# Kernel tuning notes

Hardware: AMD Instinct MI355X
Metric: run time of the kernel (lower is better)

## Reference

```python
import jax, jax.numpy as jnp
import numpy as np

MAX_SEQ = 512
HIDDEN = 1024
E = 2 * HIDDEN  # expansion
S = 128         # head dim s
EPS = 1e-5


def setup_inputs() -> dict:
    key = jax.random.key(0)
    ks = jax.random.split(key, 10)
    B, N = 32, 512
    x = jax.random.normal(ks[0], (B, N, HIDDEN), dtype=jnp.float32)
    attention_mask = jnp.ones((B, N), dtype=jnp.float32)
    gamma = jax.random.uniform(ks[1], (2, S), dtype=jnp.float32)
    beta = jax.random.uniform(ks[2], (2, S), dtype=jnp.float32)
    w = jax.random.uniform(ks[3], (2 * MAX_SEQ - 1,), dtype=jnp.float32)
    a_p = jax.random.uniform(ks[4], (1, S), dtype=jnp.float32)
    b_p = jax.random.uniform(ks[5], (1, S), dtype=jnp.float32)
    # uv: Linear(hidden -> 2e+s), stored input-major for x @ uv_w
    uv_w = jax.random.normal(ks[6], (HIDDEN, 2 * E + S), dtype=jnp.float32) * 0.02
    uv_b = jnp.zeros((2 * E + S,), dtype=jnp.float32)
    o_w = jax.random.normal(ks[7], (E, HIDDEN), dtype=jnp.float32) * 0.02
    o_b = jnp.zeros((HIDDEN,), dtype=jnp.float32)
    ln_g = jnp.ones((HIDDEN,), dtype=jnp.float32)
    ln_b = jnp.zeros((HIDDEN,), dtype=jnp.float32)
    return {"x": x, "attention_mask": attention_mask, "gamma": gamma, "beta": beta,
            "w": w, "a_p": a_p, "b_p": b_p, "uv_w": uv_w, "uv_b": uv_b,
            "o_w": o_w, "o_b": o_b, "ln_g": ln_g, "ln_b": ln_b}


def _rope_seq(x):
    # x: [b, n, 2, s]; rotary positions along axis 1 (matches module's rope(x, dim=1))
    n, d = x.shape[1], x.shape[-1]
    half = d // 2
    pos = jnp.arange(n, dtype=jnp.float32)
    # inv_freq = 10000 ** (arange(half)/half)  (freq_seq = -arange/half, inv = 10000**-freq_seq)
    inv_freq = jnp.power(10000.0, jnp.arange(half, dtype=jnp.float32) / half)
    sinusoid = pos[:, None] * inv_freq  # [n, half]
    sin = jnp.sin(sinusoid)[None, :, None, :]
    cos = jnp.cos(sinusoid)[None, :, None, :]
    x1, x2 = jnp.split(x, 2, axis=-1)
    return jnp.concatenate([x1 * cos - x2 * sin, x2 * cos + x1 * sin], axis=-1)


def _rel_pos_bias(w, seq_len):
    # Toeplitz trick (max_seq_length <= 512 path)
    t = jnp.pad(w[: 2 * MAX_SEQ - 1], (0, MAX_SEQ))          # [3S-1]
    t = jnp.tile(t, MAX_SEQ)[: -MAX_SEQ].reshape(-1, MAX_SEQ, 3 * MAX_SEQ - 2)
    r = (2 * MAX_SEQ - 1) // 2
    t = t[..., r:-r]                                          # [1, S, S]
    return t[:, :seq_len, :seq_len]


def reference(x, attention_mask, gamma, beta, w, a_p, b_p, uv_w, uv_b, o_w, o_b, ln_g, ln_b):
    n = x.shape[1]
    shortcut = x
    mu = jnp.mean(x, axis=-1, keepdims=True)
    var = jnp.mean(jnp.square(x - mu), axis=-1, keepdims=True)
    xn = (x - mu) * jax.lax.rsqrt(var + EPS) * ln_g + ln_b
    uv = jax.nn.silu(xn @ uv_w + uv_b)                        # [b, n, 2e+s]
    u, v, base = jnp.split(uv, [E, 2 * E], axis=-1)
    base = base[..., None, :] * gamma + beta                  # [b, n, 2, s]
    base = _rope_seq(base)
    q, k = base[:, :, 0], base[:, :, 1]                       # [b, n, s]
    qk = jnp.einsum('bnd,bmd->bnm', q, k)
    qk = qk + ((1.0 - attention_mask) * -1e12)[:, None, :]
    bias = _rel_pos_bias(w, n)                                # [1, n, n]
    kernel = jnp.square(jax.nn.relu(qk / MAX_SEQ + bias))
    out = u * jnp.einsum('bnm,bme->bne', kernel, v)           # [b, n, e]
    return out @ o_w + o_b + shortcut
```

## Files before the change

kernel.cpp:

```cpp
#include <hip/hip_runtime.h>
#include <math.h>

#define HIDDEN 1024
#define NSEQ   512
#define BATCH  32
#define EDIM   2048
#define SDIM   128
#define UVN    (2 * EDIM + SDIM)

using short8  = __attribute__((ext_vector_type(8))) short;
using float4x = __attribute__((ext_vector_type(4))) float;

__device__ __forceinline__ ushort f2bf(float f) {
    unsigned u = __float_as_uint(f);
    u += 0x7FFFu + ((u >> 16) & 1u);
    return (ushort)(u >> 16);
}
__device__ __forceinline__ float bf2f(ushort h) {
    return __uint_as_float(((unsigned)h) << 16);
}

#define ASYNC16(gp, lp) __builtin_amdgcn_global_load_lds( \
    (const __attribute__((address_space(1))) unsigned int*)(unsigned long long)(const void*)(gp), \
    (__attribute__((address_space(3))) unsigned int*)(unsigned int)(unsigned long long)(const void*)(lp), \
    16, 0, 0)

__global__ __launch_bounds__(64) void tab_kernel(float* __restrict__ sin_t,
                                                 float* __restrict__ cos_t) {
    int i = blockIdx.x;
    int j = threadIdx.x;
    double inv = pow(10000.0, (double)j / 64.0);
    double ang = (double)i * inv;
    sin_t[i * 64 + j] = (float)sin(ang);
    cos_t[i * 64 + j] = (float)cos(ang);
}

__global__ __launch_bounds__(256) void transpose_f32_bf16(const float* __restrict__ src,
                                                          ushort* __restrict__ dst,
                                                          int R, int Cc) {
    __shared__ float tile[32][33];
    const int bx = blockIdx.x;
    const int by = blockIdx.y;
    const int lx = threadIdx.x & 31;
    const int gy = threadIdx.x >> 5;
#pragma unroll
    for (int i = 0; i < 4; ++i) {
        int r = by * 32 + gy + i * 8;
        tile[gy + i * 8][lx] = src[(size_t)r * Cc + bx * 32 + lx];
    }
    __syncthreads();
#pragma unroll
    for (int i = 0; i < 4; ++i) {
        int c = bx * 32 + gy + i * 8;
        dst[(size_t)c * R + by * 32 + lx] = f2bf(tile[lx][gy + i * 8]);
    }
}

__global__ __launch_bounds__(256) void ln_kernel(const float* __restrict__ x,
                                                 const float* __restrict__ g,
                                                 const float* __restrict__ b,
                                                 ushort* __restrict__ xn) {
    const size_t t = blockIdx.x;
    const int tid = threadIdx.x;
    const float4 v = ((const float4*)(x + t * HIDDEN))[tid];
    float s = v.x + v.y + v.z + v.w;
#pragma unroll
    for (int off = 32; off > 0; off >>= 1) s += __shfl_down(s, off);
    __shared__ float red[4];
    const int wid = tid >> 6, lane = tid & 63;
    if (lane == 0) red[wid] = s;
    __syncthreads();
    const float mean = (red[0] + red[1] + red[2] + red[3]) * (1.0f / HIDDEN);
    __syncthreads();
    const float dx = v.x - mean, dy = v.y - mean, dz = v.z - mean, dw = v.w - mean;
    float s2 = dx * dx + dy * dy + dz * dz + dw * dw;
#pragma unroll
    for (int off = 32; off > 0; off >>= 1) s2 += __shfl_down(s2, off);
    if (lane == 0) red[wid] = s2;
    __syncthreads();
    const float var = (red[0] + red[1] + red[2] + red[3]) * (1.0f / HIDDEN);
    const float rs = rsqrtf(var + 1e-5f);
    const float4 gv = ((const float4*)g)[tid];
    const float4 bv = ((const float4*)b)[tid];
    ushort4 o;
    o.x = f2bf(dx * rs * gv.x + bv.x);
    o.y = f2bf(dy * rs * gv.y + bv.y);
    o.z = f2bf(dz * rs * gv.z + bv.z);
    o.w = f2bf(dw * rs * gv.w + bv.w);
    ((ushort4*)(xn + t * HIDDEN))[tid] = o;
}

__device__ __forceinline__ void mfma_core_128(const ushort* __restrict__ A,
                                              const ushort* __restrict__ Bt,
                                              const int lda, const int ldb, const int K,
                                              const int m0, const int n0,
                                              ushort* As, ushort* Bs,
                                              float4x (&acc)[4][4]) {
    const int tid = threadIdx.x;
    const int l = tid & 63, w = tid >> 6;
    const int wm = (w & 1) << 6, wn = (w >> 1) << 6;

    const int c0 = w * 128 + l;
    const int r0 = c0 >> 2, kc0 = (c0 & 3) * 8;
    const int c1 = c0 + 64;
    const int r1 = c1 >> 2, kc1 = (c1 & 3) * 8;
    char* ldsA0 = (char*)As + (size_t)(w * 128) * 16;
    char* ldsA1 = ldsA0 + 1024;
    char* ldsB0 = (char*)Bs + (size_t)(w * 128) * 16;
    char* ldsB1 = ldsB0 + 1024;
    const ushort* gA0 = A + (size_t)(m0 + r0) * lda + kc0;
    const ushort* gA1 = A + (size_t)(m0 + r1) * lda + kc1;
    const ushort* gB0 = Bt + (size_t)(n0 + r0) * ldb + kc0;
    const ushort* gB1 = Bt + (size_t)(n0 + r1) * ldb + kc1;

    const int lr = l & 15, lk = (l >> 4) * 8;
    int aoff[4], boff[4];
#pragma unroll
    for (int i = 0; i < 4; ++i) {
        aoff[i] = (wm + i * 16 + lr) * 32 + lk;
        boff[i] = (wn + i * 16 + lr) * 32 + lk;
    }

    for (int k0 = 0; k0 < K; k0 += 32) {
        __syncthreads();
        ASYNC16(gA0 + k0, ldsA0);
        ASYNC16(gA1 + k0, ldsA1);
        ASYNC16(gB0 + k0, ldsB0);
        ASYNC16(gB1 + k0, ldsB1);
        __syncthreads();
        short8 af[4], bfr[4];
#pragma unroll
        for (int i = 0; i < 4; ++i) af[i] = *(const short8*)(As + aoff[i]);
#pragma unroll
        for (int i = 0; i < 4; ++i) bfr[i] = *(const short8*)(Bs + boff[i]);
#pragma unroll
        for (int mi = 0; mi < 4; ++mi)
#pragma unroll
            for (int ni = 0; ni < 4; ++ni)
                acc[mi][ni] = __builtin_amdgcn_mfma_f32_16x16x32_bf16(
                    af[mi], bfr[ni], acc[mi][ni], 0, 0, 0);
    }
}

template <typename F>
__device__ __forceinline__ void epilogue_loop(const float4x (&acc)[4][4],
                                              int m0, int n0, F body) {
    const int l = threadIdx.x & 63, w = threadIdx.x >> 6;
    const int wm = (w & 1) << 6, wn = (w >> 1) << 6;
    const int lrow = (l >> 4) << 2, lcol = l & 15;
#pragma unroll
    for (int mi = 0; mi < 4; ++mi)
#pragma unroll
        for (int ni = 0; ni < 4; ++ni)
#pragma unroll
            for (int r = 0; r < 4; ++r) {
                const int m = m0 + wm + mi * 16 + lrow + r;
                const int n = n0 + wn + ni * 16 + lcol;
                body(m, n, acc[mi][ni][r]);
            }
}

__global__ __launch_bounds__(256) void gemm_uv_mfma(const ushort* __restrict__ A,
                                                    const ushort* __restrict__ Bt,
                                                    const float* __restrict__ bias,
                                                    ushort* __restrict__ U,
                                                    ushort* __restrict__ VT,
                                                    float* __restrict__ BASE) {
    __shared__ ushort As[128 * 32], Bs[128 * 32];
    float4x acc[4][4] = {};
    const int n0 = blockIdx.x * 128, m0 = blockIdx.y * 128;
    mfma_core_128(A, Bt, HIDDEN, HIDDEN, HIDDEN, m0, n0, As, Bs, acc);
    const int bx = blockIdx.x;
    if (bx < 16) {
        epilogue_loop(acc, m0, n0, [&](int m, int n, float aval) {
            float val = aval + bias[n];
            val = val / (1.0f + expf(-val));
            U[(size_t)m * EDIM + n] = f2bf(val);
        });
    } else if (bx < 32) {
        epilogue_loop(acc, m0, n0, [&](int m, int n, float aval) {
            float val = aval + bias[n];
            val = val / (1.0f + expf(-val));
            const int e = n - EDIM;
            const int b = m >> 9;
            const int s = m & (NSEQ - 1);
            VT[((size_t)b * EDIM + e) * NSEQ + s] = f2bf(val);
        });
    } else {
        epilogue_loop(acc, m0, n0, [&](int m, int n, float aval) {
            float val = aval + bias[n];
            val = val / (1.0f + expf(-val));
            BASE[(size_t)m * SDIM + (n - 2 * EDIM)] = val;
        });
    }
}

__global__ __launch_bounds__(128) void rope_kernel(const float* __restrict__ base,
                                                   const float* __restrict__ gamma,
                                                   const float* __restrict__ beta,
                                                   const float* __restrict__ sin_t,
                                                   const float* __restrict__ cos_t,
                                                   float* __restrict__ q,
                                                   float* __restrict__ k) {
    const size_t t = blockIdx.x;
    const int d = threadIdx.x;
    const int pos = (int)(t & (NSEQ - 1));
    __shared__ float vq[128], vk[128];
    const float bval = base[t * SDIM + d];
    vq[d] = bval * gamma[d] + beta[d];
    vk[d] = bval * gamma[SDIM + d] + beta[SDIM + d];
    __syncthreads();
    const int h = d & 63;
    const float sn = sin_t[pos * 64 + h];
    const float cs = cos_t[pos * 64 + h];
    float oq, ok;
    if (d < 64) {
        oq = vq[d] * cs - vq[d + 64] * sn;
        ok = vk[d] * cs - vk[d + 64] * sn;
    } else {
        oq = vq[d] * cs + vq[d - 64] * sn;
        ok = vk[d] * cs + vk[d - 64] * sn;
    }
    q[t * SDIM + d] = oq;
    k[t * SDIM + d] = ok;
}

__global__ __launch_bounds__(256) void gemm_qk(const float* __restrict__ q,
                                               const float* __restrict__ k,
                                               const float* __restrict__ mask,
                                               const float* __restrict__ w,
                                               ushort* __restrict__ km) {
    __shared__ float As[16][68];
    __shared__ float Bs[16][68];
    const int b = blockIdx.z;
    const float* A = q + (size_t)b * NSEQ * SDIM;
    const float* B = k + (size_t)b * NSEQ * SDIM;
    const int tid = threadIdx.x;
    const int tx = tid & 15, ty = tid >> 4;
    const int arow = tid >> 2, acol = (tid & 3) << 2;
    const int n0 = blockIdx.x * 64, m0 = blockIdx.y * 64;
    float acc[4][4] = {};
    for (int k0 = 0; k0 < SDIM; k0 += 16) {
        float4 av = *(const float4*)(A + (size_t)(m0 + arow) * SDIM + (k0 + acol));
        float4 bv = *(const float4*)(B + (size_t)(n0 + arow) * SDIM + (k0 + acol));
        As[acol + 0][arow] = av.x; As[acol + 1][arow] = av.y;
        As[acol + 2][arow] = av.z; As[acol + 3][arow] = av.w;
        Bs[acol + 0][arow] = bv.x; Bs[acol + 1][arow] = bv.y;
        Bs[acol + 2][arow] = bv.z; Bs[acol + 3][arow] = bv.w;
        __syncthreads();
#pragma unroll
        for (int kk = 0; kk < 16; ++kk) {
            const float4 a4 = *(const float4*)&As[kk][ty << 2];
            const float4 b4 = *(const float4*)&Bs[kk][tx << 2];
            const float a[4] = {a4.x, a4.y, a4.z, a4.w};
            const float bb[4] = {b4.x, b4.y, b4.z, b4.w};
#pragma unroll
            for (int i = 0; i < 4; ++i)
#pragma unroll
                for (int j = 0; j < 4; ++j)
                    acc[i][j] = fmaf(a[i], bb[j], acc[i][j]);
        }
        __syncthreads();
    }
    const float inv512 = 1.0f / 512.0f;
#pragma unroll
    for (int i = 0; i < 4; ++i) {
        const int ii = m0 + (ty << 2) + i;
#pragma unroll
        for (int j = 0; j < 4; ++j) {
            const int jj = n0 + (tx << 2) + j;
            const float mterm = (1.0f - mask[b * NSEQ + jj]) * -1e12f;
            float val = (acc[i][j] + mterm) * inv512 + w[511 + jj - ii];
            val = fmaxf(val, 0.0f);
            km[(size_t)b * NSEQ * NSEQ + (size_t)ii * NSEQ + jj] = f2bf(val * val);
        }
    }
}

__global__ __launch_bounds__(256) void gemm_pv_mfma(const ushort* __restrict__ km,
                                                    const ushort* __restrict__ vT,
                                                    ushort* __restrict__ ug) {
    __shared__ ushort As[128 * 32], Bs[128 * 32];
    float4x acc[4][4] = {};
    const int b = blockIdx.z;
    const int n0 = blockIdx.x * 128, m0 = blockIdx.y * 128;
    mfma_core_128(km + (size_t)b * NSEQ * NSEQ, vT + (size_t)b * EDIM * NSEQ,
                  NSEQ, NSEQ, NSEQ, m0, n0, As, Bs, acc);
    const size_t tokbase = (size_t)b * NSEQ;
    epilogue_loop(acc, m0, n0, [&](int m, int n, float aval) {
        const size_t idx = (tokbase + m) * EDIM + n;
        ug[idx] = f2bf(bf2f(ug[idx]) * aval);
    });
}

__global__ __launch_bounds__(256) void gemm_out_mfma(const ushort* __restrict__ A,
                                                     const ushort* __restrict__ Bt,
                                                     const float* __restrict__ ob,
                                                     const float* __restrict__ x,
                                                     float* __restrict__ out) {
    __shared__ ushort As[128 * 32], Bs[128 * 32];
    float4x acc[4][4] = {};
    const int n0 = blockIdx.x * 128, m0 = blockIdx.y * 128;
    mfma_core_128(A, Bt, EDIM, EDIM, EDIM, m0, n0, As, Bs, acc);
    epilogue_loop(acc, m0, n0, [&](int m, int n, float aval) {
        out[(size_t)m * HIDDEN + n] = aval + ob[n] + x[(size_t)m * HIDDEN + n];
    });
}

extern "C" void kernel_launch(void* const* d_in, const int* in_sizes, int n_in,
                              void* d_out, int out_size, void* d_ws, size_t ws_size,
                              hipStream_t stream) {
    const float* x     = (const float*)d_in[0];
    const float* mask  = (const float*)d_in[1];
    const float* gamma = (const float*)d_in[2];
    const float* beta  = (const float*)d_in[3];
    const float* w     = (const float*)d_in[4];
    const float* uv_w  = (const float*)d_in[7];
    const float* uv_b  = (const float*)d_in[8];
    const float* o_w   = (const float*)d_in[9];
    const float* o_b   = (const float*)d_in[10];
    const float* ln_g  = (const float*)d_in[11];
    const float* ln_b  = (const float*)d_in[12];
    float* out = (float*)d_out;

    int C = 32;
    while (C > 1) {
        unsigned long long need = (unsigned long long)C * 5505024ull + 13107200ull;
        if (need <= (unsigned long long)ws_size) break;
        C >>= 1;
    }
    const int R = C * NSEQ;

    char* p = (char*)d_ws;
    ushort* xn  = (ushort*)p;  p += (size_t)C * 1048576;
    ushort* u   = (ushort*)p;  p += (size_t)C * 2097152;
    ushort* vT  = (ushort*)p;  p += (size_t)C * 2097152;
    float* base = (float*)p;   p += (size_t)C * 262144;
    float* sint = (float*)p;   p += 131072;
    float* cost = (float*)p;   p += 131072;
    ushort* uv_wt = (ushort*)p; p += 8650752;
    ushort* o_wt  = (ushort*)p; p += 4194304;
    float* q  = (float*)xn;
    float* k  = (float*)((char*)xn + (size_t)C * 262144);
    ushort* km = (ushort*)((char*)xn + (size_t)C * 524288);

    hipLaunchKernelGGL(tab_kernel, dim3(512), dim3(64), 0, stream, sint, cost);
    hipLaunchKernelGGL(transpose_f32_bf16, dim3(132, 32), dim3(256), 0, stream,
                       uv_w, uv_wt, HIDDEN, UVN);
    hipLaunchKernelGGL(transpose_f32_bf16, dim3(32, 64), dim3(256), 0, stream,
                       o_w, o_wt, EDIM, HIDDEN);

    for (int b0 = 0; b0 < BATCH; b0 += C) {
        const float* xc = x + (size_t)b0 * NSEQ * HIDDEN;
        float*       oc = out + (size_t)b0 * NSEQ * HIDDEN;
        const float* mc = mask + (size_t)b0 * NSEQ;
        hipLaunchKernelGGL(ln_kernel, dim3(R), dim3(256), 0, stream, xc, ln_g, ln_b, xn);
        hipLaunchKernelGGL(gemm_uv_mfma, dim3(33, R / 128), dim3(256), 0, stream,
                           xn, uv_wt, uv_b, u, vT, base);
        hipLaunchKernelGGL(rope_kernel, dim3(R), dim3(128), 0, stream,
                           base, gamma, beta, sint, cost, q, k);
        hipLaunchKernelGGL(gemm_qk, dim3(8, 8, C), dim3(256), 0, stream, q, k, mc, w, km);
        hipLaunchKernelGGL(gemm_pv_mfma, dim3(16, 4, C), dim3(256), 0, stream, km, vT, u);
        hipLaunchKernelGGL(gemm_out_mfma, dim3(8, R / 128), dim3(256), 0, stream,
                           u, o_wt, o_b, xc, oc);
    }
}
```

Before: 607.9 us.

## Use 256x256 MFMA tiles with double-buffered async LDS pipeline for big GEMMs

Adds a 512-thread 256x256-tile bf16 MFMA core with K-step 64, double-buffered 128KB LDS, swizzled async global-to-LDS loads interleaved with four MFMA phases, and setprio hints. The UV, PV and output GEMMs switch to this core, and the small 128-column base projection is split into its own 128-tile kernel. The aim is more data reuse per LDS load and load latency hidden behind MFMA work. In exchange, the grids are much smaller (fewer blocks per launch) and register and LDS pressure rise.

```diff
diff --git a/kernel.cpp b/kernel.cpp
--- a/kernel.cpp
+++ b/kernel.cpp
@@ -160,25 +160,176 @@
             }
 }
 
-__global__ __launch_bounds__(256) void gemm_uv_mfma(const ushort* __restrict__ A,
-                                                    const ushort* __restrict__ Bt,
-                                                    const float* __restrict__ bias,
-                                                    ushort* __restrict__ U,
-                                                    ushort* __restrict__ VT,
-                                                    float* __restrict__ BASE) {
-    __shared__ ushort As[128 * 32], Bs[128 * 32];
-    float4x acc[4][4] = {};
-    const int n0 = blockIdx.x * 128, m0 = blockIdx.y * 128;
-    mfma_core_128(A, Bt, HIDDEN, HIDDEN, HIDDEN, m0, n0, As, Bs, acc);
-    const int bx = blockIdx.x;
-    if (bx < 16) {
-        epilogue_loop(acc, m0, n0, [&](int m, int n, float aval) {
+__device__ __forceinline__ void mfma_core_256(const ushort* __restrict__ A,
+                                              const ushort* __restrict__ Bt,
+                                              const int lda, const int ldb, const int K,
+                                              const int m0, const int n0,
+                                              char* smem,
+                                              float4x (&acc)[8][4]) {
+    const int tid = threadIdx.x;
+    const int l = tid & 63, w = tid >> 6;
+    const int wm = w >> 2, wn = w & 3;
+
+    const int srow = l >> 2;
+    const int kcol = (w & 1) * 32 + (((tid & 3) ^ ((l >> 3) & 3)) << 3);
+    const int rb0  = w >> 1;
+    const ushort* gA[4];
+    const ushort* gB[4];
+#pragma unroll
+    for (int j = 0; j < 4; ++j) {
+        const int row = (j * 4 + rb0) * 16 + srow;
+        gA[j] = A  + (size_t)(m0 + row) * lda + kcol;
+        gB[j] = Bt + (size_t)(n0 + row) * ldb + kcol;
+    }
+    char* const ldsA = smem;
+    char* const ldsB = smem + 65536;
+    const int wdst = w * 1024;
+
+#define STG_A(buf, j, t)  ASYNC16(gA[j] + (size_t)(t) * 64, ldsA + (buf) * 32768 + (j) * 8192 + wdst)
+#define STG_B(buf, j, t)  ASYNC16(gB[j] + (size_t)(t) * 64, ldsB + (buf) * 32768 + (j) * 8192 + wdst)
+#define RAWBAR() do { __builtin_amdgcn_sched_barrier(0); __builtin_amdgcn_s_barrier(); \
+                      __builtin_amdgcn_sched_barrier(0); } while (0)
+
+    const int LB = (l & 15) * 64 + (((l >> 4) ^ ((l >> 1) & 3)) << 4);
+    const int rbbA0 = wm * 4;
+    const int rbbA1 = 8 + wm * 4;
+    const int cbbB0 = wn * 2;
+    const int cbbB1 = 8 + wn * 2;
+
+    const int KT = K >> 6;
+
+    STG_A(0, 0, 0); STG_A(0, 1, 0); STG_A(0, 2, 0); STG_A(0, 3, 0);
+    STG_B(0, 0, 0); STG_B(0, 1, 0); STG_B(0, 2, 0); STG_B(0, 3, 0);
+    STG_A(1, 0, 1); STG_A(1, 1, 1); STG_B(1, 2, 1); STG_B(1, 3, 1);
+    asm volatile("s_waitcnt vmcnt(4)" ::: "memory");
+    RAWBAR();
+
+    for (int t = 0; t < KT; ++t) {
+        const int buf = t & 1, nbuf = buf ^ 1;
+        const char* Ab = ldsA + buf * 32768;
+        const char* Bb = ldsB + buf * 32768;
+        short8 a[4][2], bb[2][2];
+
+#pragma unroll
+        for (int mi = 0; mi < 4; ++mi) {
+            a[mi][0] = *(const short8*)(Ab + (rbbA0 + mi) * 2048 + LB);
+            a[mi][1] = *(const short8*)(Ab + (rbbA0 + mi) * 2048 + 1024 + LB);
+        }
+#pragma unroll
+        for (int ni = 0; ni < 2; ++ni) {
+            bb[ni][0] = *(const short8*)(Bb + (cbbB0 + ni) * 2048 + LB);
+            bb[ni][1] = *(const short8*)(Bb + (cbbB0 + ni) * 2048 + 1024 + LB);
+        }
+        if (t + 1 < KT) { STG_A(nbuf, 2, t + 1); STG_A(nbuf, 3, t + 1); }
+        RAWBAR();
+        __builtin_amdgcn_s_setprio(1);
+#pragma unroll
+        for (int mi = 0; mi < 4; ++mi)
+#pragma unroll
+            for (int ni = 0; ni < 2; ++ni) {
+                acc[mi][ni] = __builtin_amdgcn_mfma_f32_16x16x32_bf16(a[mi][0], bb[ni][0], acc[mi][ni], 0, 0, 0);
+                acc[mi][ni] = __builtin_amdgcn_mfma_f32_16x16x32_bf16(a[mi][1], bb[ni][1], acc[mi][ni], 0, 0, 0);
+            }
+        __builtin_amdgcn_s_setprio(0);
+        RAWBAR();
+
+#pragma unroll
+        for (int ni = 0; ni < 2; ++ni) {
+            bb[ni][0] = *(const short8*)(Bb + (cbbB1 + ni) * 2048 + LB);
+            bb[ni][1] = *(const short8*)(Bb + (cbbB1 + ni) * 2048 + 1024 + LB);
+        }
+        if (t + 1 < KT) { STG_B(nbuf, 0, t + 1); STG_B(nbuf, 1, t + 1); }
+        RAWBAR();
+        __builtin_amdgcn_s_setprio(1);
+#pragma unroll
+        for (int mi = 0; mi < 4; ++mi)
+#pragma unroll
+            for (int ni = 0; ni < 2; ++ni) {
+                acc[mi][2 + ni] = __builtin_amdgcn_mfma_f32_16x16x32_bf16(a[mi][0], bb[ni][0], acc[mi][2 + ni], 0, 0, 0);
+                acc[mi][2 + ni] = __builtin_amdgcn_mfma_f32_16x16x32_bf16(a[mi][1], bb[ni][1], acc[mi][2 + ni], 0, 0, 0);
+            }
+        __builtin_amdgcn_s_setprio(0);
+        RAWBAR();
+
+#pragma unroll
+        for (int mi = 0; mi < 4; ++mi) {
+            a[mi][0] = *(const short8*)(Ab + (rbbA1 + mi) * 2048 + LB);
+            a[mi][1] = *(const short8*)(Ab + (rbbA1 + mi) * 2048 + 1024 + LB);
+        }
+        if (t + 2 < KT) { STG_A(buf, 0, t + 2); STG_A(buf, 1, t + 2); }
+        RAWBAR();
+        __builtin_amdgcn_s_setprio(1);
+#pragma unroll
+        for (int mi = 0; mi < 4; ++mi)
+#pragma unroll
+            for (int ni = 0; ni < 2; ++ni) {
+                acc[4 + mi][2 + ni] = __builtin_amdgcn_mfma_f32_16x16x32_bf16(a[mi][0], bb[ni][0], acc[4 + mi][2 + ni], 0, 0, 0);
+                acc[4 + mi][2 + ni] = __builtin_amdgcn_mfma_f32_16x16x32_bf16(a[mi][1], bb[ni][1], acc[4 + mi][2 + ni], 0, 0, 0);
+            }
+        __builtin_amdgcn_s_setprio(0);
+        RAWBAR();
+
+#pragma unroll
+        for (int ni = 0; ni < 2; ++ni) {
+            bb[ni][0] = *(const short8*)(Bb + (cbbB0 + ni) * 2048 + LB);
+            bb[ni][1] = *(const short8*)(Bb + (cbbB0 + ni) * 2048 + 1024 + LB);
+        }
+        if (t + 2 < KT) { STG_B(buf, 2, t + 2); STG_B(buf, 3, t + 2); }
+        __builtin_amdgcn_sched_barrier(0);
+        __builtin_amdgcn_s_setprio(1);
+#pragma unroll
+        for (int mi = 0; mi < 4; ++mi)
+#pragma unroll
+            for (int ni = 0; ni < 2; ++ni) {
+                acc[4 + mi][ni] = __builtin_amdgcn_mfma_f32_16x16x32_bf16(a[mi][0], bb[ni][0], acc[4 + mi][ni], 0, 0, 0);
+                acc[4 + mi][ni] = __builtin_amdgcn_mfma_f32_16x16x32_bf16(a[mi][1], bb[ni][1], acc[4 + mi][ni], 0, 0, 0);
+            }
+        __builtin_amdgcn_s_setprio(0);
+        if (t + 2 < KT) asm volatile("s_waitcnt vmcnt(4)" ::: "memory");
+        else            asm volatile("s_waitcnt vmcnt(0)" ::: "memory");
+        RAWBAR();
+    }
+#undef STG_A
+#undef STG_B
+#undef RAWBAR
+}
+
+template <typename F>
+__device__ __forceinline__ void epilogue_256(const float4x (&acc)[8][4],
+                                             int m0, int n0, F body) {
+    const int tid = threadIdx.x;
+    const int l = tid & 63, w = tid >> 6;
+    const int wm = w >> 2, wn = w & 3;
+    const int lrow = (l >> 4) << 2, lcol = l & 15;
+#pragma unroll
+    for (int i = 0; i < 8; ++i)
+#pragma unroll
+        for (int j = 0; j < 4; ++j)
+#pragma unroll
+            for (int r = 0; r < 4; ++r) {
+                const int m = m0 + (i >> 2) * 128 + wm * 64 + (i & 3) * 16 + lrow + r;
+                const int n = n0 + (j >> 1) * 128 + wn * 32 + (j & 1) * 16 + lcol;
+                body(m, n, acc[i][j][r]);
+            }
+}
+
+__global__ __launch_bounds__(512) void gemm_uv2(const ushort* __restrict__ A,
+                                                const ushort* __restrict__ Bt,
+                                                const float* __restrict__ bias,
+                                                ushort* __restrict__ U,
+                                                ushort* __restrict__ VT) {
+    __shared__ __align__(16) char smem[131072];
+    float4x acc[8][4] = {};
+    const int n0 = blockIdx.x * 256, m0 = blockIdx.y * 256;
+    mfma_core_256(A, Bt, HIDDEN, HIDDEN, HIDDEN, m0, n0, smem, acc);
+    if (blockIdx.x < 8) {
+        epilogue_256(acc, m0, n0, [&](int m, int n, float aval) {
             float val = aval + bias[n];
             val = val / (1.0f + expf(-val));
             U[(size_t)m * EDIM + n] = f2bf(val);
         });
-    } else if (bx < 32) {
-        epilogue_loop(acc, m0, n0, [&](int m, int n, float aval) {
+    } else {
+        epilogue_256(acc, m0, n0, [&](int m, int n, float aval) {
             float val = aval + bias[n];
             val = val / (1.0f + expf(-val));
             const int e = n - EDIM;
@@ -186,13 +337,23 @@
             const int s = m & (NSEQ - 1);
             VT[((size_t)b * EDIM + e) * NSEQ + s] = f2bf(val);
         });
-    } else {
-        epilogue_loop(acc, m0, n0, [&](int m, int n, float aval) {
-            float val = aval + bias[n];
-            val = val / (1.0f + expf(-val));
-            BASE[(size_t)m * SDIM + (n - 2 * EDIM)] = val;
-        });
-    }
+    }
+}
+
+__global__ __launch_bounds__(256) void gemm_base_mfma(const ushort* __restrict__ A,
+                                                      const ushort* __restrict__ Bt,
+                                                      const float* __restrict__ bias,
+                                                      float* __restrict__ BASE) {
+    __shared__ ushort As[128 * 32], Bs[128 * 32];
+    float4x acc[4][4] = {};
+    const int n0 = 2 * EDIM;
+    const int m0 = blockIdx.y * 128;
+    mfma_core_128(A, Bt, HIDDEN, HIDDEN, HIDDEN, m0, n0, As, Bs, acc);
+    epilogue_loop(acc, m0, n0, [&](int m, int n, float aval) {
+        float val = aval + bias[n];
+        val = val / (1.0f + expf(-val));
+        BASE[(size_t)m * SDIM + (n - 2 * EDIM)] = val;
+    });
 }
 
 __global__ __launch_bounds__(128) void rope_kernel(const float* __restrict__ base,
@@ -253,12 +414,12 @@
             const float4 a4 = *(const float4*)&As[kk][ty << 2];
             const float4 b4 = *(const float4*)&Bs[kk][tx << 2];
             const float a[4] = {a4.x, a4.y, a4.z, a4.w};
-            const float bb[4] = {b4.x, b4.y, b4.z, b4.w};
+            const float bbv[4] = {b4.x, b4.y, b4.z, b4.w};
 #pragma unroll
             for (int i = 0; i < 4; ++i)
 #pragma unroll
                 for (int j = 0; j < 4; ++j)
-                    acc[i][j] = fmaf(a[i], bb[j], acc[i][j]);
+                    acc[i][j] = fmaf(a[i], bbv[j], acc[i][j]);
         }
         __syncthreads();
     }
@@ -277,32 +438,32 @@
     }
 }
 
-__global__ __launch_bounds__(256) void gemm_pv_mfma(const ushort* __restrict__ km,
-                                                    const ushort* __restrict__ vT,
-                                                    ushort* __restrict__ ug) {
-    __shared__ ushort As[128 * 32], Bs[128 * 32];
-    float4x acc[4][4] = {};
+__global__ __launch_bounds__(512) void gemm_pv2(const ushort* __restrict__ km,
+                                                const ushort* __restrict__ vT,
+                                                ushort* __restrict__ ug) {
+    __shared__ __align__(16) char smem[131072];
+    float4x acc[8][4] = {};
     const int b = blockIdx.z;
-    const int n0 = blockIdx.x * 128, m0 = blockIdx.y * 128;
-    mfma_core_128(km + (size_t)b * NSEQ * NSEQ, vT + (size_t)b * EDIM * NSEQ,
-                  NSEQ, NSEQ, NSEQ, m0, n0, As, Bs, acc);
+    const int n0 = blockIdx.x * 256, m0 = blockIdx.y * 256;
+    mfma_core_256(km + (size_t)b * NSEQ * NSEQ, vT + (size_t)b * EDIM * NSEQ,
+                  NSEQ, NSEQ, NSEQ, m0, n0, smem, acc);
     const size_t tokbase = (size_t)b * NSEQ;
-    epilogue_loop(acc, m0, n0, [&](int m, int n, float aval) {
+    epilogue_256(acc, m0, n0, [&](int m, int n, float aval) {
         const size_t idx = (tokbase + m) * EDIM + n;
         ug[idx] = f2bf(bf2f(ug[idx]) * aval);
     });
 }
 
-__global__ __launch_bounds__(256) void gemm_out_mfma(const ushort* __restrict__ A,
-                                                     const ushort* __restrict__ Bt,
-                                                     const float* __restrict__ ob,
-                                                     const float* __restrict__ x,
-                                                     float* __restrict__ out) {
-    __shared__ ushort As[128 * 32], Bs[128 * 32];
-    float4x acc[4][4] = {};
-    const int n0 = blockIdx.x * 128, m0 = blockIdx.y * 128;
-    mfma_core_128(A, Bt, EDIM, EDIM, EDIM, m0, n0, As, Bs, acc);
-    epilogue_loop(acc, m0, n0, [&](int m, int n, float aval) {
+__global__ __launch_bounds__(512) void gemm_out2(const ushort* __restrict__ A,
+                                                 const ushort* __restrict__ Bt,
+                                                 const float* __restrict__ ob,
+                                                 const float* __restrict__ x,
+                                                 float* __restrict__ out) {
+    __shared__ __align__(16) char smem[131072];
+    float4x acc[8][4] = {};
+    const int n0 = blockIdx.x * 256, m0 = blockIdx.y * 256;
+    mfma_core_256(A, Bt, EDIM, EDIM, EDIM, m0, n0, smem, acc);
+    epilogue_256(acc, m0, n0, [&](int m, int n, float aval) {
         out[(size_t)m * HIDDEN + n] = aval + ob[n] + x[(size_t)m * HIDDEN + n];
     });
 }
@@ -355,13 +516,15 @@
         float*       oc = out + (size_t)b0 * NSEQ * HIDDEN;
         const float* mc = mask + (size_t)b0 * NSEQ;
         hipLaunchKernelGGL(ln_kernel, dim3(R), dim3(256), 0, stream, xc, ln_g, ln_b, xn);
-        hipLaunchKernelGGL(gemm_uv_mfma, dim3(33, R / 128), dim3(256), 0, stream,
-                           xn, uv_wt, uv_b, u, vT, base);
+        hipLaunchKernelGGL(gemm_uv2, dim3(16, R / 256), dim3(512), 0, stream,
+                           xn, uv_wt, uv_b, u, vT);
+        hipLaunchKernelGGL(gemm_base_mfma, dim3(1, R / 128), dim3(256), 0, stream,
+                           xn, uv_wt, uv_b, base);
         hipLaunchKernelGGL(rope_kernel, dim3(R), dim3(128), 0, stream,
                            base, gamma, beta, sint, cost, q, k);
         hipLaunchKernelGGL(gemm_qk, dim3(8, 8, C), dim3(256), 0, stream, q, k, mc, w, km);
-        hipLaunchKernelGGL(gemm_pv_mfma, dim3(16, 4, C), dim3(256), 0, stream, km, vT, u);
-        hipLaunchKernelGGL(gemm_out_mfma, dim3(8, R / 128), dim3(256), 0, stream,
+        hipLaunchKernelGGL(gemm_pv2, dim3(8, 2, C), dim3(512), 0, stream, km, vT, u);
+        hipLaunchKernelGGL(gemm_out2, dim3(4, R / 256), dim3(512), 0, stream,
                            u, o_wt, o_b, xc, oc);
     }
 }
```

Result: faster. 556.7 us (-8.4%).

## Use 256x256 double-buffered async-LDS MFMA tiles for the large GEMMs

Applied to the files above, without the earlier changes.

Adds a new GEMM core with 256x256 output tiles per 1024-thread block. It double-buffers 64-wide K slices in 128 KB of LDS using async global-to-LDS loads with a swizzled layout, and raises wave priority around the MFMA bursts. The uv, pv and output GEMMs move to this core, which raises data reuse per load and overlaps loading with compute. The small base projection is split into its own 128-tile kernel. The large LDS footprint limits each CU to one block, so fewer blocks run concurrently and tail effects on the smaller grids may grow.

```diff
diff --git a/kernel.cpp b/kernel.cpp
--- a/kernel.cpp
+++ b/kernel.cpp
@@ -160,25 +160,105 @@
             }
 }
 
-__global__ __launch_bounds__(256) void gemm_uv_mfma(const ushort* __restrict__ A,
+__device__ __forceinline__ void mfma_core_v3(const ushort* __restrict__ A,
+                                             const ushort* __restrict__ Bt,
+                                             const int lda, const int ldb, const int K,
+                                             const int m0, const int n0,
+                                             char* smem,
+                                             float4x (&acc)[4][4]) {
+    const int tid = threadIdx.x;
+    const int l = tid & 63, w = tid >> 6;
+    const int wm = w >> 2, wn = w & 3;
+
+    const int srow = l >> 2;
+    const int kswz = ((l & 3) ^ ((l >> 3) & 3)) << 3;
+    const ushort* gA = A + (size_t)(m0 + w * 16 + srow) * lda + kswz;
+    const ushort* gB = Bt + (size_t)(n0 + w * 16 + srow) * ldb + kswz;
+    char* const ldsA = smem;
+    char* const ldsB = smem + 65536;
+    const int woff = w * 2048;
+
+    const int LB = (l & 15) * 64 + (((l >> 4) ^ ((l >> 1) & 3)) << 4);
+    const int rbb = wm * 4, cbb = wn * 4;
+    const int KT = K >> 6;
+
+    ASYNC16(gA, ldsA + woff);
+    ASYNC16(gA + 32, ldsA + woff + 1024);
+    ASYNC16(gB, ldsB + woff);
+    ASYNC16(gB + 32, ldsB + woff + 1024);
+    __syncthreads();
+
+    for (int t = 0; t < KT; ++t) {
+        const int buf = t & 1;
+        const char* Ab = ldsA + buf * 32768;
+        const char* Bb = ldsB + buf * 32768;
+        if (t + 1 < KT) {
+            const size_t g = (size_t)(t + 1) * 64;
+            char* dA = ldsA + (buf ^ 1) * 32768 + woff;
+            char* dB = ldsB + (buf ^ 1) * 32768 + woff;
+            ASYNC16(gA + g, dA);
+            ASYNC16(gA + g + 32, dA + 1024);
+            ASYNC16(gB + g, dB);
+            ASYNC16(gB + g + 32, dB + 1024);
+        }
+        __builtin_amdgcn_sched_barrier(0);
+#pragma unroll
+        for (int kh = 0; kh < 2; ++kh) {
+            short8 a[4], b[4];
+#pragma unroll
+            for (int i = 0; i < 4; ++i) {
+                a[i] = *(const short8*)(Ab + (rbb + i) * 2048 + kh * 1024 + LB);
+                b[i] = *(const short8*)(Bb + (cbb + i) * 2048 + kh * 1024 + LB);
+            }
+            __builtin_amdgcn_s_setprio(1);
+#pragma unroll
+            for (int i = 0; i < 4; ++i)
+#pragma unroll
+                for (int j = 0; j < 4; ++j)
+                    acc[i][j] = __builtin_amdgcn_mfma_f32_16x16x32_bf16(
+                        a[i], b[j], acc[i][j], 0, 0, 0);
+            __builtin_amdgcn_s_setprio(0);
+        }
+        __syncthreads();
+    }
+}
+
+template <typename F>
+__device__ __forceinline__ void epilogue_v3(const float4x (&acc)[4][4],
+                                            int m0, int n0, F body) {
+    const int tid = threadIdx.x;
+    const int l = tid & 63, w = tid >> 6;
+    const int wm = w >> 2, wn = w & 3;
+    const int lrow = (l >> 4) << 2, lcol = l & 15;
+#pragma unroll
+    for (int i = 0; i < 4; ++i)
+#pragma unroll
+        for (int j = 0; j < 4; ++j)
+#pragma unroll
+            for (int r = 0; r < 4; ++r) {
+                const int m = m0 + wm * 64 + i * 16 + lrow + r;
+                const int n = n0 + wn * 64 + j * 16 + lcol;
+                body(m, n, acc[i][j][r]);
+            }
+}
+
+__global__ __launch_bounds__(1024, 4) void gemm_uv3(const ushort* __restrict__ A,
                                                     const ushort* __restrict__ Bt,
                                                     const float* __restrict__ bias,
                                                     ushort* __restrict__ U,
-                                                    ushort* __restrict__ VT,
-                                                    float* __restrict__ BASE) {
-    __shared__ ushort As[128 * 32], Bs[128 * 32];
+                                                    ushort* __restrict__ VT) {
+    __shared__ __align__(16) char smem[131072];
     float4x acc[4][4] = {};
-    const int n0 = blockIdx.x * 128, m0 = blockIdx.y * 128;
-    mfma_core_128(A, Bt, HIDDEN, HIDDEN, HIDDEN, m0, n0, As, Bs, acc);
-    const int bx = blockIdx.x;
-    if (bx < 16) {
-        epilogue_loop(acc, m0, n0, [&](int m, int n, float aval) {
+    const int n0 = blockIdx.x * 256, m0 = blockIdx.y * 256;
+    mfma_core_v3(A, Bt, HIDDEN, HIDDEN, HIDDEN, m0, n0, smem, acc);
+    if (blockIdx.x < 8) {
+        epilogue_v3(acc, m0, n0, [&](int m, int n, float aval) {
             float val = aval + bias[n];
             val = val / (1.0f + expf(-val));
             U[(size_t)m * EDIM + n] = f2bf(val);
         });
-    } else if (bx < 32) {
-        epilogue_loop(acc, m0, n0, [&](int m, int n, float aval) {
+    } else {
+        epilogue_v3(acc, m0, n0, [&](int m, int n, float aval) {
             float val = aval + bias[n];
             val = val / (1.0f + expf(-val));
             const int e = n - EDIM;
@@ -186,13 +266,23 @@
             const int s = m & (NSEQ - 1);
             VT[((size_t)b * EDIM + e) * NSEQ + s] = f2bf(val);
         });
-    } else {
-        epilogue_loop(acc, m0, n0, [&](int m, int n, float aval) {
-            float val = aval + bias[n];
-            val = val / (1.0f + expf(-val));
-            BASE[(size_t)m * SDIM + (n - 2 * EDIM)] = val;
-        });
-    }
+    }
+}
+
+__global__ __launch_bounds__(256) void gemm_base_mfma(const ushort* __restrict__ A,
+                                                      const ushort* __restrict__ Bt,
+                                                      const float* __restrict__ bias,
+                                                      float* __restrict__ BASE) {
+    __shared__ ushort As[128 * 32], Bs[128 * 32];
+    float4x acc[4][4] = {};
+    const int n0 = 2 * EDIM;
+    const int m0 = blockIdx.y * 128;
+    mfma_core_128(A, Bt, HIDDEN, HIDDEN, HIDDEN, m0, n0, As, Bs, acc);
+    epilogue_loop(acc, m0, n0, [&](int m, int n, float aval) {
+        float val = aval + bias[n];
+        val = val / (1.0f + expf(-val));
+        BASE[(size_t)m * SDIM + (n - 2 * EDIM)] = val;
+    });
 }
 
 __global__ __launch_bounds__(128) void rope_kernel(const float* __restrict__ base,
@@ -253,12 +343,12 @@
             const float4 a4 = *(const float4*)&As[kk][ty << 2];
             const float4 b4 = *(const float4*)&Bs[kk][tx << 2];
             const float a[4] = {a4.x, a4.y, a4.z, a4.w};
-            const float bb[4] = {b4.x, b4.y, b4.z, b4.w};
+            const float bbv[4] = {b4.x, b4.y, b4.z, b4.w};
 #pragma unroll
             for (int i = 0; i < 4; ++i)
 #pragma unroll
                 for (int j = 0; j < 4; ++j)
-                    acc[i][j] = fmaf(a[i], bb[j], acc[i][j]);
+                    acc[i][j] = fmaf(a[i], bbv[j], acc[i][j]);
         }
         __syncthreads();
     }
@@ -277,32 +367,32 @@
     }
 }
 
-__global__ __launch_bounds__(256) void gemm_pv_mfma(const ushort* __restrict__ km,
+__global__ __launch_bounds__(1024, 4) void gemm_pv3(const ushort* __restrict__ km,
                                                     const ushort* __restrict__ vT,
                                                     ushort* __restrict__ ug) {
-    __shared__ ushort As[128 * 32], Bs[128 * 32];
+    __shared__ __align__(16) char smem[131072];
     float4x acc[4][4] = {};
     const int b = blockIdx.z;
-    const int n0 = blockIdx.x * 128, m0 = blockIdx.y * 128;
-    mfma_core_128(km + (size_t)b * NSEQ * NSEQ, vT + (size_t)b * EDIM * NSEQ,
-                  NSEQ, NSEQ, NSEQ, m0, n0, As, Bs, acc);
+    const int n0 = blockIdx.x * 256, m0 = blockIdx.y * 256;
+    mfma_core_v3(km + (size_t)b * NSEQ * NSEQ, vT + (size_t)b * EDIM * NSEQ,
+                 NSEQ, NSEQ, NSEQ, m0, n0, smem, acc);
     const size_t tokbase = (size_t)b * NSEQ;
-    epilogue_loop(acc, m0, n0, [&](int m, int n, float aval) {
+    epilogue_v3(acc, m0, n0, [&](int m, int n, float aval) {
         const size_t idx = (tokbase + m) * EDIM + n;
         ug[idx] = f2bf(bf2f(ug[idx]) * aval);
     });
 }
 
-__global__ __launch_bounds__(256) void gemm_out_mfma(const ushort* __restrict__ A,
+__global__ __launch_bounds__(1024, 4) void gemm_out3(const ushort* __restrict__ A,
                                                      const ushort* __restrict__ Bt,
                                                      const float* __restrict__ ob,
                                                      const float* __restrict__ x,
                                                      float* __restrict__ out) {
-    __shared__ ushort As[128 * 32], Bs[128 * 32];
+    __shared__ __align__(16) char smem[131072];
     float4x acc[4][4] = {};
-    const int n0 = blockIdx.x * 128, m0 = blockIdx.y * 128;
-    mfma_core_128(A, Bt, EDIM, EDIM, EDIM, m0, n0, As, Bs, acc);
-    epilogue_loop(acc, m0, n0, [&](int m, int n, float aval) {
+    const int n0 = blockIdx.x * 256, m0 = blockIdx.y * 256;
+    mfma_core_v3(A, Bt, EDIM, EDIM, EDIM, m0, n0, smem, acc);
+    epilogue_v3(acc, m0, n0, [&](int m, int n, float aval) {
         out[(size_t)m * HIDDEN + n] = aval + ob[n] + x[(size_t)m * HIDDEN + n];
     });
 }
@@ -355,13 +445,15 @@
         float*       oc = out + (size_t)b0 * NSEQ * HIDDEN;
         const float* mc = mask + (size_t)b0 * NSEQ;
         hipLaunchKernelGGL(ln_kernel, dim3(R), dim3(256), 0, stream, xc, ln_g, ln_b, xn);
-        hipLaunchKernelGGL(gemm_uv_mfma, dim3(33, R / 128), dim3(256), 0, stream,
-                           xn, uv_wt, uv_b, u, vT, base);
+        hipLaunchKernelGGL(gemm_uv3, dim3(16, R / 256), dim3(1024), 0, stream,
+                           xn, uv_wt, uv_b, u, vT);
+        hipLaunchKernelGGL(gemm_base_mfma, dim3(1, R / 128), dim3(256), 0, stream,
+                           xn, uv_wt, uv_b, base);
         hipLaunchKernelGGL(rope_kernel, dim3(R), dim3(128), 0, stream,
                            base, gamma, beta, sint, cost, q, k);
         hipLaunchKernelGGL(gemm_qk, dim3(8, 8, C), dim3(256), 0, stream, q, k, mc, w, km);
-        hipLaunchKernelGGL(gemm_pv_mfma, dim3(16, 4, C), dim3(256), 0, stream, km, vT, u);
-        hipLaunchKernelGGL(gemm_out_mfma, dim3(8, R / 128), dim3(256), 0, stream,
+        hipLaunchKernelGGL(gemm_pv3, dim3(8, 2, C), dim3(1024), 0, stream, km, vT, u);
+        hipLaunchKernelGGL(gemm_out3, dim3(4, R / 256), dim3(1024), 0, stream,
                            u, o_wt, o_b, xc, oc);
     }
 }
```

Result: faster. 532.2 us (-12.4%).

## Double-buffer MFMA GEMM core with swizzled LDS layout and wave priority

Applied to the files above, without the earlier changes.

Replaces the shared GEMM mainloop with a double-buffered version that issues async global-to-LDS loads for the next K tile while MFMAs run on the current one, cutting one barrier per iteration. The LDS layout is XOR-swizzled to reduce bank conflicts on the fragment reads, and s_setprio raises wave priority around the MFMA block. Launch bounds now request 4 blocks per CU, and LDS per block doubles to 32 KB.

```diff
diff --git a/kernel.cpp b/kernel.cpp
--- a/kernel.cpp
+++ b/kernel.cpp
@@ -90,95 +90,101 @@
     ((ushort4*)(xn + t * HIDDEN))[tid] = o;
 }
 
-__device__ __forceinline__ void mfma_core_128(const ushort* __restrict__ A,
-                                              const ushort* __restrict__ Bt,
-                                              const int lda, const int ldb, const int K,
-                                              const int m0, const int n0,
-                                              ushort* As, ushort* Bs,
-                                              float4x (&acc)[4][4]) {
+__device__ __forceinline__ void mfma_core_v4(const ushort* __restrict__ A,
+                                             const ushort* __restrict__ Bt,
+                                             const int lda, const int ldb, const int K,
+                                             const int m0, const int n0,
+                                             char* smem,
+                                             float4x (&acc)[4][4]) {
     const int tid = threadIdx.x;
     const int l = tid & 63, w = tid >> 6;
-    const int wm = (w & 1) << 6, wn = (w >> 1) << 6;
-
-    const int c0 = w * 128 + l;
-    const int r0 = c0 >> 2, kc0 = (c0 & 3) * 8;
-    const int c1 = c0 + 64;
-    const int r1 = c1 >> 2, kc1 = (c1 & 3) * 8;
-    char* ldsA0 = (char*)As + (size_t)(w * 128) * 16;
-    char* ldsA1 = ldsA0 + 1024;
-    char* ldsB0 = (char*)Bs + (size_t)(w * 128) * 16;
-    char* ldsB1 = ldsB0 + 1024;
-    const ushort* gA0 = A + (size_t)(m0 + r0) * lda + kc0;
-    const ushort* gA1 = A + (size_t)(m0 + r1) * lda + kc1;
-    const ushort* gB0 = Bt + (size_t)(n0 + r0) * ldb + kc0;
-    const ushort* gB1 = Bt + (size_t)(n0 + r1) * ldb + kc1;
-
-    const int lr = l & 15, lk = (l >> 4) * 8;
-    int aoff[4], boff[4];
-#pragma unroll
-    for (int i = 0; i < 4; ++i) {
-        aoff[i] = (wm + i * 16 + lr) * 32 + lk;
-        boff[i] = (wn + i * 16 + lr) * 32 + lk;
-    }
-
-    for (int k0 = 0; k0 < K; k0 += 32) {
+    const int wm = w & 1, wn = w >> 1;
+
+    const int srow = l >> 2;
+    const int kswz = ((l & 3) ^ ((l >> 3) & 3)) << 3;
+    const ushort* gA0 = A + (size_t)(m0 + w * 16 + srow) * lda + kswz;
+    const ushort* gA1 = A + (size_t)(m0 + (w + 4) * 16 + srow) * lda + kswz;
+    const ushort* gB0 = Bt + (size_t)(n0 + w * 16 + srow) * ldb + kswz;
+    const ushort* gB1 = Bt + (size_t)(n0 + (w + 4) * 16 + srow) * ldb + kswz;
+
+    const int LB = (l & 15) * 64 + (((l >> 4) ^ ((l >> 1) & 3)) << 4);
+    const int KT = K >> 5;
+
+    ASYNC16(gA0, smem + w * 1024);
+    ASYNC16(gA1, smem + (4 + w) * 1024);
+    ASYNC16(gB0, smem + 8192 + w * 1024);
+    ASYNC16(gB1, smem + 8192 + (4 + w) * 1024);
+    __syncthreads();
+
+    for (int t = 0; t < KT; ++t) {
+        const int buf = t & 1;
+        const char* Ab = smem + buf * 16384;
+        const char* Bb = Ab + 8192;
+        if (t + 1 < KT) {
+            const size_t g = (size_t)(t + 1) * 32;
+            char* d = smem + (buf ^ 1) * 16384;
+            ASYNC16(gA0 + g, d + w * 1024);
+            ASYNC16(gA1 + g, d + (4 + w) * 1024);
+            ASYNC16(gB0 + g, d + 8192 + w * 1024);
+            ASYNC16(gB1 + g, d + 8192 + (4 + w) * 1024);
+        }
+        __builtin_amdgcn_sched_barrier(0);
+        short8 a[4], b[4];
+#pragma unroll
+        for (int i = 0; i < 4; ++i) {
+            a[i] = *(const short8*)(Ab + (wm * 4 + i) * 1024 + LB);
+            b[i] = *(const short8*)(Bb + (wn * 4 + i) * 1024 + LB);
+        }
+        __builtin_amdgcn_s_setprio(1);
+#pragma unroll
+        for (int i = 0; i < 4; ++i)
+#pragma unroll
+            for (int j = 0; j < 4; ++j)
+                acc[i][j] = __builtin_amdgcn_mfma_f32_16x16x32_bf16(
+                    a[i], b[j], acc[i][j], 0, 0, 0);
+        __builtin_amdgcn_s_setprio(0);
         __syncthreads();
-        ASYNC16(gA0 + k0, ldsA0);
-        ASYNC16(gA1 + k0, ldsA1);
-        ASYNC16(gB0 + k0, ldsB0);
-        ASYNC16(gB1 + k0, ldsB1);
-        __syncthreads();
-        short8 af[4], bfr[4];
-#pragma unroll
-        for (int i = 0; i < 4; ++i) af[i] = *(const short8*)(As + aoff[i]);
-#pragma unroll
-        for (int i = 0; i < 4; ++i) bfr[i] = *(const short8*)(Bs + boff[i]);
-#pragma unroll
-        for (int mi = 0; mi < 4; ++mi)
-#pragma unroll
-            for (int ni = 0; ni < 4; ++ni)
-                acc[mi][ni] = __builtin_amdgcn_mfma_f32_16x16x32_bf16(
-                    af[mi], bfr[ni], acc[mi][ni], 0, 0, 0);
     }
 }
 
 template <typename F>
-__device__ __forceinline__ void epilogue_loop(const float4x (&acc)[4][4],
-                                              int m0, int n0, F body) {
-    const int l = threadIdx.x & 63, w = threadIdx.x >> 6;
-    const int wm = (w & 1) << 6, wn = (w >> 1) << 6;
+__device__ __forceinline__ void epilogue_v4(const float4x (&acc)[4][4],
+                                            int m0, int n0, F body) {
+    const int tid = threadIdx.x;
+    const int l = tid & 63, w = tid >> 6;
+    const int wm = w & 1, wn = w >> 1;
     const int lrow = (l >> 4) << 2, lcol = l & 15;
 #pragma unroll
-    for (int mi = 0; mi < 4; ++mi)
-#pragma unroll
-        for (int ni = 0; ni < 4; ++ni)
+    for (int i = 0; i < 4; ++i)
+#pragma unroll
+        for (int j = 0; j < 4; ++j)
 #pragma unroll
             for (int r = 0; r < 4; ++r) {
-                const int m = m0 + wm + mi * 16 + lrow + r;
-                const int n = n0 + wn + ni * 16 + lcol;
-                body(m, n, acc[mi][ni][r]);
+                const int m = m0 + wm * 64 + i * 16 + lrow + r;
+                const int n = n0 + wn * 64 + j * 16 + lcol;
+                body(m, n, acc[i][j][r]);
             }
 }
 
-__global__ __launch_bounds__(256) void gemm_uv_mfma(const ushort* __restrict__ A,
-                                                    const ushort* __restrict__ Bt,
-                                                    const float* __restrict__ bias,
-                                                    ushort* __restrict__ U,
-                                                    ushort* __restrict__ VT,
-                                                    float* __restrict__ BASE) {
-    __shared__ ushort As[128 * 32], Bs[128 * 32];
+__global__ __launch_bounds__(256, 4) void gemm_uv4(const ushort* __restrict__ A,
+                                                   const ushort* __restrict__ Bt,
+                                                   const float* __restrict__ bias,
+                                                   ushort* __restrict__ U,
+                                                   ushort* __restrict__ VT,
+                                                   float* __restrict__ BASE) {
+    __shared__ __align__(16) char smem[32768];
     float4x acc[4][4] = {};
     const int n0 = blockIdx.x * 128, m0 = blockIdx.y * 128;
-    mfma_core_128(A, Bt, HIDDEN, HIDDEN, HIDDEN, m0, n0, As, Bs, acc);
+    mfma_core_v4(A, Bt, HIDDEN, HIDDEN, HIDDEN, m0, n0, smem, acc);
     const int bx = blockIdx.x;
     if (bx < 16) {
-        epilogue_loop(acc, m0, n0, [&](int m, int n, float aval) {
+        epilogue_v4(acc, m0, n0, [&](int m, int n, float aval) {
             float val = aval + bias[n];
             val = val / (1.0f + expf(-val));
             U[(size_t)m * EDIM + n] = f2bf(val);
         });
     } else if (bx < 32) {
-        epilogue_loop(acc, m0, n0, [&](int m, int n, float aval) {
+        epilogue_v4(acc, m0, n0, [&](int m, int n, float aval) {
             float val = aval + bias[n];
             val = val / (1.0f + expf(-val));
             const int e = n - EDIM;
@@ -187,7 +193,7 @@
             VT[((size_t)b * EDIM + e) * NSEQ + s] = f2bf(val);
         });
     } else {
-        epilogue_loop(acc, m0, n0, [&](int m, int n, float aval) {
+        epilogue_v4(acc, m0, n0, [&](int m, int n, float aval) {
             float val = aval + bias[n];
             val = val / (1.0f + expf(-val));
             BASE[(size_t)m * SDIM + (n - 2 * EDIM)] = val;
@@ -253,12 +259,12 @@
             const float4 a4 = *(const float4*)&As[kk][ty << 2];
             const float4 b4 = *(const float4*)&Bs[kk][tx << 2];
             const float a[4] = {a4.x, a4.y, a4.z, a4.w};
-            const float bb[4] = {b4.x, b4.y, b4.z, b4.w};
+            const float bbv[4] = {b4.x, b4.y, b4.z, b4.w};
 #pragma unroll
             for (int i = 0; i < 4; ++i)
 #pragma unroll
                 for (int j = 0; j < 4; ++j)
-                    acc[i][j] = fmaf(a[i], bb[j], acc[i][j]);
+                    acc[i][j] = fmaf(a[i], bbv[j], acc[i][j]);
         }
         __syncthreads();
     }
@@ -277,32 +283,32 @@
     }
 }
 
-__global__ __launch_bounds__(256) void gemm_pv_mfma(const ushort* __restrict__ km,
-                                                    const ushort* __restrict__ vT,
-                                                    ushort* __restrict__ ug) {
-    __shared__ ushort As[128 * 32], Bs[128 * 32];
+__global__ __launch_bounds__(256, 4) void gemm_pv4(const ushort* __restrict__ km,
+                                                   const ushort* __restrict__ vT,
+                                                   ushort* __restrict__ ug) {
+    __shared__ __align__(16) char smem[32768];
     float4x acc[4][4] = {};
     const int b = blockIdx.z;
     const int n0 = blockIdx.x * 128, m0 = blockIdx.y * 128;
-    mfma_core_128(km + (size_t)b * NSEQ * NSEQ, vT + (size_t)b * EDIM * NSEQ,
-                  NSEQ, NSEQ, NSEQ, m0, n0, As, Bs, acc);
+    mfma_core_v4(km + (size_t)b * NSEQ * NSEQ, vT + (size_t)b * EDIM * NSEQ,
+                 NSEQ, NSEQ, NSEQ, m0, n0, smem, acc);
     const size_t tokbase = (size_t)b * NSEQ;
-    epilogue_loop(acc, m0, n0, [&](int m, int n, float aval) {
+    epilogue_v4(acc, m0, n0, [&](int m, int n, float aval) {
         const size_t idx = (tokbase + m) * EDIM + n;
         ug[idx] = f2bf(bf2f(ug[idx]) * aval);
     });
 }
 
-__global__ __launch_bounds__(256) void gemm_out_mfma(const ushort* __restrict__ A,
-                                                     const ushort* __restrict__ Bt,
-                                                     const float* __restrict__ ob,
-                                                     const float* __restrict__ x,
-                                                     float* __restrict__ out) {
-    __shared__ ushort As[128 * 32], Bs[128 * 32];
+__global__ __launch_bounds__(256, 4) void gemm_out4(const ushort* __restrict__ A,
+                                                    const ushort* __restrict__ Bt,
+                                                    const float* __restrict__ ob,
+                                                    const float* __restrict__ x,
+                                                    float* __restrict__ out) {
+    __shared__ __align__(16) char smem[32768];
     float4x acc[4][4] = {};
     const int n0 = blockIdx.x * 128, m0 = blockIdx.y * 128;
-    mfma_core_128(A, Bt, EDIM, EDIM, EDIM, m0, n0, As, Bs, acc);
-    epilogue_loop(acc, m0, n0, [&](int m, int n, float aval) {
+    mfma_core_v4(A, Bt, EDIM, EDIM, EDIM, m0, n0, smem, acc);
+    epilogue_v4(acc, m0, n0, [&](int m, int n, float aval) {
         out[(size_t)m * HIDDEN + n] = aval + ob[n] + x[(size_t)m * HIDDEN + n];
     });
 }
@@ -355,13 +361,13 @@
         float*       oc = out + (size_t)b0 * NSEQ * HIDDEN;
         const float* mc = mask + (size_t)b0 * NSEQ;
         hipLaunchKernelGGL(ln_kernel, dim3(R), dim3(256), 0, stream, xc, ln_g, ln_b, xn);
-        hipLaunchKernelGGL(gemm_uv_mfma, dim3(33, R / 128), dim3(256), 0, stream,
+        hipLaunchKernelGGL(gemm_uv4, dim3(33, R / 128), dim3(256), 0, stream,
                            xn, uv_wt, uv_b, u, vT, base);
         hipLaunchKernelGGL(rope_kernel, dim3(R), dim3(128), 0, stream,
                            base, gamma, beta, sint, cost, q, k);
         hipLaunchKernelGGL(gemm_qk, dim3(8, 8, C), dim3(256), 0, stream, q, k, mc, w, km);
-        hipLaunchKernelGGL(gemm_pv_mfma, dim3(16, 4, C), dim3(256), 0, stream, km, vT, u);
-        hipLaunchKernelGGL(gemm_out_mfma, dim3(8, R / 128), dim3(256), 0, stream,
+        hipLaunchKernelGGL(gemm_pv4, dim3(16, 4, C), dim3(256), 0, stream, km, vT, u);
+        hipLaunchKernelGGL(gemm_out4, dim3(8, R / 128), dim3(256), 0, stream,
                            u, o_wt, o_b, xc, oc);
     }
 }
```

New measurement: 598.9 us. About the same (-1.5%).
